# Performance work log

Measured on AMD Instinct MI355X. Metric: run time of the kernel, lower is better.

## Reference

```python
import jax, jax.numpy as jnp
import numpy as np

B, C, L = 16, 256, 2048


def setup_inputs() -> dict:
    key = jax.random.key(0)
    ks = jax.random.split(key, 7)
    s = 0.05
    return {
        "x": jax.random.normal(ks[0], (B, C, L), dtype=jnp.float32),
        "W_theta": jax.random.normal(ks[1], (C, C), dtype=jnp.float32) * s,
        "b_theta": jax.random.normal(ks[2], (C,), dtype=jnp.float32) * s,
        "W_phi": jax.random.normal(ks[3], (C, C), dtype=jnp.float32) * s,
        "b_phi": jax.random.normal(ks[4], (C,), dtype=jnp.float32) * s,
        "W_g": jax.random.normal(ks[5], (C, C), dtype=jnp.float32) * s,
        "b_g": jax.random.normal(ks[6], (C,), dtype=jnp.float32) * s,
    }


def reference(x, W_theta, b_theta, W_phi, b_phi, W_g, b_g):
    # x: [B, C, L]; 1x1 Conv1d == linear over channel dim: out[b,o,l] = W[o,c] x[b,c,l] + b[o]
    q = jnp.einsum('oc,bcl->bol', W_theta, x) + b_theta[None, :, None]  # [B,C,L]
    k = jnp.einsum('oc,bcl->bol', W_phi, x) + b_phi[None, :, None]
    v = jnp.einsum('oc,bcl->bol', W_g, x) + b_g[None, :, None]
    num_c = x.shape[1]
    # scores[b,i,j] = sum_c q[b,c,i] * k[b,c,j]
    scores = jnp.einsum('bci,bcj->bij', q, k) / jnp.sqrt(jnp.float32(num_c))  # [B,L,L]
    attn = jax.nn.softmax(scores, axis=-1)
    # out[b,i,c] = sum_j attn[b,i,j] v[b,c,j]; then permute back to [B,C,L]
    attn_out = jnp.einsum('bij,bcj->bci', attn, v)  # [B,C,L]
    return x + attn_out
```

## Files before the change

### kernel.cpp

```cpp
#include <hip/hip_runtime.h>
#include <math.h>

#define B_ 16
#define C_ 256
#define L_ 2048

using short8 = __attribute__((ext_vector_type(8))) short;
using f32x4  = __attribute__((ext_vector_type(4))) float;
using f32x16 = __attribute__((ext_vector_type(16))) float;
typedef unsigned int uint;

__device__ __forceinline__ unsigned short f2bf(float f) {
  unsigned u = __float_as_uint(f);
  return (unsigned short)((u + 0x7FFFu + ((u >> 16) & 1u)) >> 16);
}

__device__ __forceinline__ void gload16(const void* src, void* dst) {
  __builtin_amdgcn_global_load_lds(
      (const __attribute__((address_space(1))) unsigned int*)src,
      (__attribute__((address_space(3))) unsigned int*)dst, 16, 0, 0);
}

__global__ __launch_bounds__(256) void convert_w(const float* __restrict__ wt,
                                                 const float* __restrict__ wp,
                                                 const float* __restrict__ wg,
                                                 unsigned short* __restrict__ dst) {
  int i = blockIdx.x * 256 + threadIdx.x;
  dst[i]          = f2bf(wt[i]);
  dst[65536 + i]  = f2bf(wp[i]);
  dst[131072 + i] = f2bf(wg[i]);
}

__global__ __launch_bounds__(256, 2) void proj_kernel(
    const float* __restrict__ x, const unsigned short* __restrict__ wbf,
    const float* __restrict__ bth, const float* __restrict__ bph,
    const float* __restrict__ bg,
    unsigned short* __restrict__ qT, unsigned short* __restrict__ kT,
    unsigned short* __restrict__ vv)
{
  const int tid  = threadIdx.x;
  const int w    = tid >> 6;
  const int lane = tid & 63;
  const int r    = lane & 15;
  const int g    = lane >> 4;
  const int l0   = blockIdx.x * 64;
  const int b    = blockIdx.y;
  const int p    = blockIdx.z;

  __shared__ unsigned short xs[64 * 64];
  __shared__ unsigned short wsd[256 * 64];

  const unsigned short* wsrc = wbf + p * 65536;

  f32x4 acc[4][4];
#pragma unroll
  for (int mi = 0; mi < 4; ++mi)
#pragma unroll
    for (int ni = 0; ni < 4; ++ni) acc[mi][ni] = f32x4{0.f, 0.f, 0.f, 0.f};

  for (int ks = 0; ks < 4; ++ks) {
    __syncthreads();
#pragma unroll
    for (int it = 0; it < 8; ++it) {
      int d  = it * 256 + w * 64 + lane;
      int o  = d >> 3;
      int cs = d & 7;
      const unsigned short* src = wsrc + o * C_ + ks * 64 + ((cs ^ (o & 7)) << 3);
      gload16(src, (void*)(wsd + (size_t)(it * 256 + w * 64) * 8));
    }
#pragma unroll
    for (int it = 0; it < 16; ++it) {
      int l = (tid & 15) + 16 * (it & 3);
      int c = (tid >> 4) + 16 * (it >> 2);
      float xvv = x[((size_t)b * C_ + ks * 64 + c) * L_ + l0 + l];
      xs[l * 64 + (((c >> 3) ^ (l & 7)) << 3) + (c & 7)] = f2bf(xvv);
    }
    __syncthreads();

#pragma unroll
    for (int kk2 = 0; kk2 < 2; ++kk2) {
      short8 xf[4], wf[4];
#pragma unroll
      for (int i = 0; i < 4; ++i) {
        int lrow = 16 * i + r;
        xf[i] = *(const short8*)(xs + lrow * 64 + (((kk2 * 4 + g) ^ (lrow & 7)) << 3));
        int orow = 64 * w + 16 * i + r;
        wf[i] = *(const short8*)(wsd + orow * 64 + (((kk2 * 4 + g) ^ (orow & 7)) << 3));
      }
      if (p < 2) {
#pragma unroll
        for (int mi = 0; mi < 4; ++mi)
#pragma unroll
          for (int ni = 0; ni < 4; ++ni)
            acc[mi][ni] = __builtin_amdgcn_mfma_f32_16x16x32_bf16(xf[mi], wf[ni], acc[mi][ni], 0, 0, 0);
      } else {
#pragma unroll
        for (int mi = 0; mi < 4; ++mi)
#pragma unroll
          for (int ni = 0; ni < 4; ++ni)
            acc[mi][ni] = __builtin_amdgcn_mfma_f32_16x16x32_bf16(wf[mi], xf[ni], acc[mi][ni], 0, 0, 0);
      }
    }
  }

  if (p < 2) {
    unsigned short* dst = (p == 0) ? qT : kT;
    const float* bias   = (p == 0) ? bth : bph;
    const float scale   = (p == 0) ? 0.09016844005556021f : 1.0f;
#pragma unroll
    for (int ni = 0; ni < 4; ++ni) {
      int o    = 64 * w + 16 * ni + r;
      float bv = bias[o];
#pragma unroll
      for (int mi = 0; mi < 4; ++mi)
#pragma unroll
        for (int rr = 0; rr < 4; ++rr) {
          int l = l0 + 16 * mi + 4 * g + rr;
          dst[((size_t)b * L_ + l) * C_ + o] = f2bf((acc[mi][ni][rr] + bv) * scale);
        }
    }
  } else {
#pragma unroll
    for (int mi = 0; mi < 4; ++mi)
#pragma unroll
      for (int rr = 0; rr < 4; ++rr) {
        int o    = 64 * w + 16 * mi + 4 * g + rr;
        float bv = bg[o];
#pragma unroll
        for (int ni = 0; ni < 4; ++ni) {
          int l = l0 + 16 * ni + r;
          vv[((size_t)b * C_ + o) * L_ + l] = f2bf(acc[mi][ni][rr] + bv);
        }
      }
  }
}

__global__ __launch_bounds__(256, 2) void attn_kernel(
    const unsigned short* __restrict__ qT, const unsigned short* __restrict__ kT,
    const unsigned short* __restrict__ vv,
    const float* __restrict__ x, float* __restrict__ out)
{
  const int tid  = threadIdx.x;
  const int w    = tid >> 6;
  const int lane = tid & 63;
  const int l31  = lane & 31;
  const int hi   = lane >> 5;
  const int ih   = w >> 1;
  const int jh   = w & 1;

  int wg = ((blockIdx.x & 7) << 6) | (blockIdx.x >> 3);
  const int i0 = (wg & 31) * 64;
  const int b  = wg >> 5;

  __shared__ unsigned short kls[64 * 256];
  __shared__ unsigned short pls[64 * 64];
  __shared__ float lsums2[2][64];

  short8 qf[16];
  const unsigned short* qrow_p = qT + ((size_t)b * L_ + i0 + 32 * ih + l31) * C_;
#pragma unroll
  for (int ks = 0; ks < 16; ++ks)
    qf[ks] = *(const short8*)(qrow_p + ks * 16 + 8 * hi);

  f32x16 oacc[2][2];
#pragma unroll
  for (int it = 0; it < 2; ++it)
#pragma unroll
    for (int ct = 0; ct < 2; ++ct)
#pragma unroll
      for (int e = 0; e < 16; ++e) oacc[it][ct][e] = 0.f;
  float lsum = 0.f;

  const unsigned short* kTb = kT + (size_t)b * L_ * C_;
  const unsigned short* vvb = vv + (size_t)b * C_ * L_;

#pragma unroll
  for (int it = 0; it < 8; ++it) {
    int d   = it * 256 + w * 64 + lane;
    int row = d >> 5;
    int cs  = d & 31;
    gload16(kTb + (size_t)row * C_ + ((cs ^ (row & 7)) << 3),
            (void*)(kls + (size_t)(it * 256 + w * 64) * 8));
  }

  for (int jt = 0; jt < 32; ++jt) {
    const int j0 = jt * 64;
    __syncthreads();

    short8 vfr[2][4];
#pragma unroll
    for (int ct = 0; ct < 2; ++ct) {
      const unsigned short* vrow = vvb + (size_t)(l31 + 32 * ct + 64 * w) * L_ + j0 + 8 * hi;
#pragma unroll
      for (int ks = 0; ks < 4; ++ks)
        vfr[ct][ks] = *(const short8*)(vrow + 16 * ks);
    }

    f32x16 sacc;
#pragma unroll
    for (int e = 0; e < 16; ++e) sacc[e] = 0.f;
    const int jrow = l31 + 32 * jh;
#pragma unroll
    for (int ks = 0; ks < 16; ++ks) {
      short8 kf = *(const short8*)(kls + jrow * 256 + (((2 * ks + hi) ^ (jrow & 7)) << 3));
      sacc = __builtin_amdgcn_mfma_f32_32x32x16_bf16(kf, qf[ks], sacc, 0, 0, 0);
    }

    {
      const int i = l31 + 32 * ih;
#pragma unroll
      for (int q = 0; q < 4; ++q) {
        float p0 = exp2f(sacc[4 * q + 0]);
        float p1 = exp2f(sacc[4 * q + 1]);
        float p2 = exp2f(sacc[4 * q + 2]);
        float p3 = exp2f(sacc[4 * q + 3]);
        lsum += (p0 + p1) + (p2 + p3);
        uint2 d2;
        d2.x = (uint)f2bf(p0) | ((uint)f2bf(p1) << 16);
        d2.y = (uint)f2bf(p2) | ((uint)f2bf(p3) << 16);
        int slot = (4 * jh + q) ^ (i & 7);
        *(uint2*)(pls + i * 64 + slot * 8 + 4 * hi) = d2;
      }
    }
    __syncthreads();

    if (jt < 31) {
#pragma unroll
      for (int it = 0; it < 8; ++it) {
        int d   = it * 256 + w * 64 + lane;
        int row = d >> 5;
        int cs  = d & 31;
        gload16(kTb + (size_t)(j0 + 64 + row) * C_ + ((cs ^ (row & 7)) << 3),
                (void*)(kls + (size_t)(it * 256 + w * 64) * 8));
      }
    }

#pragma unroll
    for (int ks = 0; ks < 4; ++ks) {
      short8 pf[2];
#pragma unroll
      for (int it = 0; it < 2; ++it) {
        int irow = l31 + 32 * it;
        pf[it] = *(const short8*)(pls + irow * 64 + (((2 * ks + hi) ^ (irow & 7)) << 3));
      }
#pragma unroll
      for (int it = 0; it < 2; ++it)
#pragma unroll
        for (int ct = 0; ct < 2; ++ct)
          oacc[it][ct] = __builtin_amdgcn_mfma_f32_32x32x16_bf16(pf[it], vfr[ct][ks], oacc[it][ct], 0, 0, 0);
    }
  }

  lsum += __shfl_xor(lsum, 32);
  if (lane < 32) lsums2[jh][32 * ih + l31] = lsum;
  __syncthreads();

#pragma unroll
  for (int it = 0; it < 2; ++it)
#pragma unroll
    for (int q = 0; q < 4; ++q) {
      int ib = 32 * it + 8 * q + 4 * hi;
      f32x4 ls0 = *(const f32x4*)(&lsums2[0][ib]);
      f32x4 ls1 = *(const f32x4*)(&lsums2[1][ib]);
      f32x4 linv;
#pragma unroll
      for (int rr = 0; rr < 4; ++rr) linv[rr] = 1.0f / (ls0[rr] + ls1[rr]);
#pragma unroll
      for (int ct = 0; ct < 2; ++ct) {
        int c = l31 + 32 * ct + 64 * w;
        size_t base = ((size_t)b * C_ + c) * L_ + i0 + ib;
        f32x4 xv = *(const f32x4*)(x + base);
        f32x4 ov;
#pragma unroll
        for (int rr = 0; rr < 4; ++rr)
          ov[rr] = xv[rr] + oacc[it][ct][4 * q + rr] * linv[rr];
        *(f32x4*)(out + base) = ov;
      }
    }
}

extern "C" void kernel_launch(void* const* d_in, const int* in_sizes, int n_in,
                              void* d_out, int out_size, void* d_ws, size_t ws_size,
                              hipStream_t stream) {
  (void)in_sizes; (void)n_in; (void)out_size; (void)ws_size;
  const float* x   = (const float*)d_in[0];
  const float* wt  = (const float*)d_in[1];
  const float* bt  = (const float*)d_in[2];
  const float* wp  = (const float*)d_in[3];
  const float* bp  = (const float*)d_in[4];
  const float* wg  = (const float*)d_in[5];
  const float* bgg = (const float*)d_in[6];
  float* out = (float*)d_out;

  char* ws = (char*)d_ws;
  unsigned short* wbf = (unsigned short*)ws;
  unsigned short* qT  = (unsigned short*)(ws + 393216);
  unsigned short* kT  = (unsigned short*)(ws + 393216 + 16777216);
  unsigned short* vv  = (unsigned short*)(ws + 393216 + 2 * 16777216);

  convert_w<<<dim3(256), dim3(256), 0, stream>>>(wt, wp, wg, wbf);
  proj_kernel<<<dim3(32, 16, 3), dim3(256), 0, stream>>>(x, wbf, bt, bp, bgg, qT, kT, vv);
  attn_kernel<<<dim3(512), dim3(256), 0, stream>>>(qT, kT, vv, x, out);
}
```

Measured before the change: 147.0 us.

## Double-buffer K tiles in attention and fuse QKV projections into one block

The attention kernel now double-buffers the K tile in LDS, so the load of the next tile is issued at the top of each iteration and no longer waits behind the softmax barrier. It also splits the score MFMA chain into two independent accumulators, precomputes the swizzled LDS addresses, uses the hardware exp and packed bf16 convert instructions, and raises wave priority around the MFMA sections. The projection kernel loads an x tile once as bf16 into LDS and loops over the three weight matrices inside a block, replacing the three-way grid split. This cuts the number of x reads but leaves only 512 projection blocks and uses more LDS per block.

```diff
diff --git a/kernel.cpp b/kernel.cpp
--- a/kernel.cpp
+++ b/kernel.cpp
@@ -1,5 +1,4 @@
 #include <hip/hip_runtime.h>
-#include <math.h>
 
 #define B_ 16
 #define C_ 256
@@ -45,93 +44,94 @@
   const int g    = lane >> 4;
   const int l0   = blockIdx.x * 64;
   const int b    = blockIdx.y;
-  const int p    = blockIdx.z;
-
-  __shared__ unsigned short xs[64 * 64];
+
+  __shared__ unsigned short xs[64 * 256];
   __shared__ unsigned short wsd[256 * 64];
 
-  const unsigned short* wsrc = wbf + p * 65536;
+#pragma unroll
+  for (int it = 0; it < 64; ++it) {
+    int l = (tid & 15) + 16 * (it & 3);
+    int c = (tid >> 4) + 16 * (it >> 2);
+    float xvv = x[((size_t)b * C_ + c) * L_ + l0 + l];
+    xs[l * 256 + (((c >> 3) ^ (l & 7)) << 3) + (c & 7)] = f2bf(xvv);
+  }
 
   f32x4 acc[4][4];
-#pragma unroll
-  for (int mi = 0; mi < 4; ++mi)
-#pragma unroll
-    for (int ni = 0; ni < 4; ++ni) acc[mi][ni] = f32x4{0.f, 0.f, 0.f, 0.f};
-
-  for (int ks = 0; ks < 4; ++ks) {
-    __syncthreads();
-#pragma unroll
-    for (int it = 0; it < 8; ++it) {
-      int d  = it * 256 + w * 64 + lane;
-      int o  = d >> 3;
-      int cs = d & 7;
-      const unsigned short* src = wsrc + o * C_ + ks * 64 + ((cs ^ (o & 7)) << 3);
-      gload16(src, (void*)(wsd + (size_t)(it * 256 + w * 64) * 8));
-    }
-#pragma unroll
-    for (int it = 0; it < 16; ++it) {
-      int l = (tid & 15) + 16 * (it & 3);
-      int c = (tid >> 4) + 16 * (it >> 2);
-      float xvv = x[((size_t)b * C_ + ks * 64 + c) * L_ + l0 + l];
-      xs[l * 64 + (((c >> 3) ^ (l & 7)) << 3) + (c & 7)] = f2bf(xvv);
-    }
-    __syncthreads();
-
-#pragma unroll
-    for (int kk2 = 0; kk2 < 2; ++kk2) {
-      short8 xf[4], wf[4];
-#pragma unroll
-      for (int i = 0; i < 4; ++i) {
-        int lrow = 16 * i + r;
-        xf[i] = *(const short8*)(xs + lrow * 64 + (((kk2 * 4 + g) ^ (lrow & 7)) << 3));
-        int orow = 64 * w + 16 * i + r;
-        wf[i] = *(const short8*)(wsd + orow * 64 + (((kk2 * 4 + g) ^ (orow & 7)) << 3));
+  for (int p = 0; p < 3; ++p) {
+    const unsigned short* wsrc = wbf + p * 65536;
+#pragma unroll
+    for (int mi = 0; mi < 4; ++mi)
+#pragma unroll
+      for (int ni = 0; ni < 4; ++ni) acc[mi][ni] = f32x4{0.f, 0.f, 0.f, 0.f};
+
+    for (int ks = 0; ks < 4; ++ks) {
+      __syncthreads();
+#pragma unroll
+      for (int it = 0; it < 8; ++it) {
+        int o  = it * 32 + (tid >> 3);
+        int cs = tid & 7;
+        gload16(wsrc + o * C_ + ks * 64 + ((cs ^ (o & 7)) << 3),
+                (void*)(wsd + (size_t)(it * 256 + w * 64) * 8));
       }
-      if (p < 2) {
-#pragma unroll
-        for (int mi = 0; mi < 4; ++mi)
-#pragma unroll
-          for (int ni = 0; ni < 4; ++ni)
-            acc[mi][ni] = __builtin_amdgcn_mfma_f32_16x16x32_bf16(xf[mi], wf[ni], acc[mi][ni], 0, 0, 0);
-      } else {
-#pragma unroll
-        for (int mi = 0; mi < 4; ++mi)
-#pragma unroll
-          for (int ni = 0; ni < 4; ++ni)
-            acc[mi][ni] = __builtin_amdgcn_mfma_f32_16x16x32_bf16(wf[mi], xf[ni], acc[mi][ni], 0, 0, 0);
+      __syncthreads();
+
+#pragma unroll
+      for (int kk2 = 0; kk2 < 2; ++kk2) {
+        short8 xf[4], wf[4];
+#pragma unroll
+        for (int i = 0; i < 4; ++i) {
+          int lrow = 16 * i + r;
+          xf[i] = *(const short8*)(xs + lrow * 256 +
+                                   (((8 * ks + 4 * kk2 + g) ^ (lrow & 7)) << 3));
+          int orow = 64 * w + 16 * i + r;
+          wf[i] = *(const short8*)(wsd + orow * 64 + (((kk2 * 4 + g) ^ (orow & 7)) << 3));
+        }
+        if (p < 2) {
+#pragma unroll
+          for (int mi = 0; mi < 4; ++mi)
+#pragma unroll
+            for (int ni = 0; ni < 4; ++ni)
+              acc[mi][ni] = __builtin_amdgcn_mfma_f32_16x16x32_bf16(xf[mi], wf[ni], acc[mi][ni], 0, 0, 0);
+        } else {
+#pragma unroll
+          for (int mi = 0; mi < 4; ++mi)
+#pragma unroll
+            for (int ni = 0; ni < 4; ++ni)
+              acc[mi][ni] = __builtin_amdgcn_mfma_f32_16x16x32_bf16(wf[mi], xf[ni], acc[mi][ni], 0, 0, 0);
+        }
       }
     }
-  }
-
-  if (p < 2) {
-    unsigned short* dst = (p == 0) ? qT : kT;
-    const float* bias   = (p == 0) ? bth : bph;
-    const float scale   = (p == 0) ? 0.09016844005556021f : 1.0f;
-#pragma unroll
-    for (int ni = 0; ni < 4; ++ni) {
-      int o    = 64 * w + 16 * ni + r;
-      float bv = bias[o];
+
+    if (p < 2) {
+      unsigned short* dst = (p == 0) ? qT : kT;
+      const float* bias   = (p == 0) ? bth : bph;
+      const float scale   = (p == 0) ? 0.09016844005556021f : 1.0f;
+#pragma unroll
+      for (int ni = 0; ni < 4; ++ni) {
+        int o    = 64 * w + 16 * ni + r;
+        float bv = bias[o];
+#pragma unroll
+        for (int mi = 0; mi < 4; ++mi)
+#pragma unroll
+          for (int rr = 0; rr < 4; ++rr) {
+            int l = l0 + 16 * mi + 4 * g + rr;
+            dst[((size_t)b * L_ + l) * C_ + o] = f2bf((acc[mi][ni][rr] + bv) * scale);
+          }
+      }
+    } else {
 #pragma unroll
       for (int mi = 0; mi < 4; ++mi)
 #pragma unroll
         for (int rr = 0; rr < 4; ++rr) {
-          int l = l0 + 16 * mi + 4 * g + rr;
-          dst[((size_t)b * L_ + l) * C_ + o] = f2bf((acc[mi][ni][rr] + bv) * scale);
+          int o    = 64 * w + 16 * mi + 4 * g + rr;
+          float bv = bg[o];
+#pragma unroll
+          for (int ni = 0; ni < 4; ++ni) {
+            int l = l0 + 16 * ni + r;
+            vv[((size_t)b * C_ + o) * L_ + l] = f2bf(acc[mi][ni][rr] + bv);
+          }
         }
     }
-  } else {
-#pragma unroll
-    for (int mi = 0; mi < 4; ++mi)
-#pragma unroll
-      for (int rr = 0; rr < 4; ++rr) {
-        int o    = 64 * w + 16 * mi + 4 * g + rr;
-        float bv = bg[o];
-#pragma unroll
-        for (int ni = 0; ni < 4; ++ni) {
-          int l = l0 + 16 * ni + r;
-          vv[((size_t)b * C_ + o) * L_ + l] = f2bf(acc[mi][ni][rr] + bv);
-        }
-      }
   }
 }
 
@@ -152,9 +152,14 @@
   const int i0 = (wg & 31) * 64;
   const int b  = wg >> 5;
 
-  __shared__ unsigned short kls[64 * 256];
+  __shared__ unsigned short kls[2][64 * 256];
   __shared__ unsigned short pls[64 * 64];
   __shared__ float lsums2[2][64];
+  unsigned short* klsf = &kls[0][0];
+  unsigned short* plsf = pls;
+
+  const unsigned short* kTb = kT + (size_t)b * L_ * C_;
+  const unsigned short* vvb = vv + (size_t)b * C_ * L_;
 
   short8 qf[16];
   const unsigned short* qrow_p = qT + ((size_t)b * L_ + i0 + 32 * ih + l31) * C_;
@@ -162,6 +167,31 @@
   for (int ks = 0; ks < 16; ++ks)
     qf[ks] = *(const short8*)(qrow_p + ks * 16 + 8 * hi);
 
+  const int jrow = l31 + 32 * jh;
+  int kfa[16];
+#pragma unroll
+  for (int k2 = 0; k2 < 8; ++k2) {
+    kfa[2 * k2]     = jrow * 256 + (((4 * k2 + hi) ^ (jrow & 7)) << 3);
+    kfa[2 * k2 + 1] = jrow * 256 + (((4 * k2 + 2 + hi) ^ (jrow & 7)) << 3);
+  }
+  int pfa[8];
+#pragma unroll
+  for (int ks = 0; ks < 4; ++ks)
+#pragma unroll
+    for (int it = 0; it < 2; ++it)
+      pfa[2 * ks + it] = (l31 + 32 * it) * 64 + (((2 * ks + hi) ^ (l31 & 7)) << 3);
+  int pwa[4];
+  {
+    const int i = l31 + 32 * ih;
+#pragma unroll
+    for (int q = 0; q < 4; ++q)
+      pwa[q] = i * 64 + (((4 * jh + q) ^ (i & 7)) << 3) + 4 * hi;
+  }
+  const int koff0 = (tid >> 5) * 256 + (((tid & 31) ^ ((tid >> 5) & 7)) << 3);
+  int voff[2];
+#pragma unroll
+  for (int ct = 0; ct < 2; ++ct) voff[ct] = (l31 + 32 * ct + 64 * w) * L_ + 8 * hi;
+
   f32x16 oacc[2][2];
 #pragma unroll
   for (int it = 0; it < 2; ++it)
@@ -171,85 +201,83 @@
       for (int e = 0; e < 16; ++e) oacc[it][ct][e] = 0.f;
   float lsum = 0.f;
 
-  const unsigned short* kTb = kT + (size_t)b * L_ * C_;
-  const unsigned short* vvb = vv + (size_t)b * C_ * L_;
-
-#pragma unroll
-  for (int it = 0; it < 8; ++it) {
-    int d   = it * 256 + w * 64 + lane;
-    int row = d >> 5;
-    int cs  = d & 31;
-    gload16(kTb + (size_t)row * C_ + ((cs ^ (row & 7)) << 3),
-            (void*)(kls + (size_t)(it * 256 + w * 64) * 8));
-  }
-
-  for (int jt = 0; jt < 32; ++jt) {
-    const int j0 = jt * 64;
-    __syncthreads();
-
-    short8 vfr[2][4];
-#pragma unroll
-    for (int ct = 0; ct < 2; ++ct) {
-      const unsigned short* vrow = vvb + (size_t)(l31 + 32 * ct + 64 * w) * L_ + j0 + 8 * hi;
-#pragma unroll
-      for (int ks = 0; ks < 4; ++ks)
-        vfr[ct][ks] = *(const short8*)(vrow + 16 * ks);
-    }
-
-    f32x16 sacc;
-#pragma unroll
-    for (int e = 0; e < 16; ++e) sacc[e] = 0.f;
-    const int jrow = l31 + 32 * jh;
-#pragma unroll
-    for (int ks = 0; ks < 16; ++ks) {
-      short8 kf = *(const short8*)(kls + jrow * 256 + (((2 * ks + hi) ^ (jrow & 7)) << 3));
-      sacc = __builtin_amdgcn_mfma_f32_32x32x16_bf16(kf, qf[ks], sacc, 0, 0, 0);
-    }
-
-    {
-      const int i = l31 + 32 * ih;
-#pragma unroll
-      for (int q = 0; q < 4; ++q) {
-        float p0 = exp2f(sacc[4 * q + 0]);
-        float p1 = exp2f(sacc[4 * q + 1]);
-        float p2 = exp2f(sacc[4 * q + 2]);
-        float p3 = exp2f(sacc[4 * q + 3]);
-        lsum += (p0 + p1) + (p2 + p3);
-        uint2 d2;
-        d2.x = (uint)f2bf(p0) | ((uint)f2bf(p1) << 16);
-        d2.y = (uint)f2bf(p2) | ((uint)f2bf(p3) << 16);
-        int slot = (4 * jh + q) ^ (i & 7);
-        *(uint2*)(pls + i * 64 + slot * 8 + 4 * hi) = d2;
-      }
-    }
-    __syncthreads();
-
-    if (jt < 31) {
-#pragma unroll
-      for (int it = 0; it < 8; ++it) {
-        int d   = it * 256 + w * 64 + lane;
-        int row = d >> 5;
-        int cs  = d & 31;
-        gload16(kTb + (size_t)(j0 + 64 + row) * C_ + ((cs ^ (row & 7)) << 3),
-                (void*)(kls + (size_t)(it * 256 + w * 64) * 8));
-      }
-    }
-
-#pragma unroll
-    for (int ks = 0; ks < 4; ++ks) {
-      short8 pf[2];
-#pragma unroll
-      for (int it = 0; it < 2; ++it) {
-        int irow = l31 + 32 * it;
-        pf[it] = *(const short8*)(pls + irow * 64 + (((2 * ks + hi) ^ (irow & 7)) << 3));
-      }
-#pragma unroll
-      for (int it = 0; it < 2; ++it)
-#pragma unroll
-        for (int ct = 0; ct < 2; ++ct)
-          oacc[it][ct] = __builtin_amdgcn_mfma_f32_32x32x16_bf16(pf[it], vfr[ct][ks], oacc[it][ct], 0, 0, 0);
-    }
-  }
+  {
+    const unsigned short* ksrc = kTb + koff0;
+#pragma unroll
+    for (int it = 0; it < 8; ++it)
+      gload16(ksrc + it * 2048, (void*)(klsf + (it * 256 + w * 64) * 8));
+  }
+  const unsigned short* kstage = kTb + 16384;
+  const unsigned short* vbase  = vvb;
+
+#define TILE_BODY(CUR, NXT, DOSTAGE)                                               \
+  {                                                                                \
+    __syncthreads();                                                               \
+    short8 vfr[2][4];                                                              \
+    _Pragma("unroll")                                                              \
+    for (int ct = 0; ct < 2; ++ct) {                                               \
+      _Pragma("unroll")                                                            \
+      for (int ks = 0; ks < 4; ++ks)                                               \
+        vfr[ct][ks] = *(const short8*)(vbase + voff[ct] + 16 * ks);                \
+    }                                                                              \
+    if (DOSTAGE) {                                                                 \
+      const unsigned short* ksrc = kstage + koff0;                                 \
+      _Pragma("unroll")                                                            \
+      for (int it = 0; it < 8; ++it)                                               \
+        gload16(ksrc + it * 2048, (void*)(klsf + (NXT) + (it * 256 + w * 64) * 8));\
+    }                                                                              \
+    f32x16 sacc0, sacc1;                                                           \
+    _Pragma("unroll")                                                              \
+    for (int e = 0; e < 16; ++e) { sacc0[e] = 0.f; sacc1[e] = 0.f; }               \
+    __builtin_amdgcn_s_setprio(1);                                                 \
+    _Pragma("unroll")                                                              \
+    for (int k2 = 0; k2 < 8; ++k2) {                                               \
+      short8 kf0 = *(const short8*)(klsf + (CUR) + kfa[2 * k2]);                   \
+      short8 kf1 = *(const short8*)(klsf + (CUR) + kfa[2 * k2 + 1]);               \
+      sacc0 = __builtin_amdgcn_mfma_f32_32x32x16_bf16(kf0, qf[2 * k2], sacc0, 0, 0, 0);      \
+      sacc1 = __builtin_amdgcn_mfma_f32_32x32x16_bf16(kf1, qf[2 * k2 + 1], sacc1, 0, 0, 0);  \
+    }                                                                              \
+    __builtin_amdgcn_s_setprio(0);                                                 \
+    _Pragma("unroll")                                                              \
+    for (int q = 0; q < 4; ++q) {                                                  \
+      float s0 = sacc0[4 * q + 0] + sacc1[4 * q + 0];                              \
+      float s1 = sacc0[4 * q + 1] + sacc1[4 * q + 1];                              \
+      float s2 = sacc0[4 * q + 2] + sacc1[4 * q + 2];                              \
+      float s3 = sacc0[4 * q + 3] + sacc1[4 * q + 3];                              \
+      float p0, p1, p2, p3;                                                        \
+      asm("v_exp_f32 %0, %1" : "=v"(p0) : "v"(s0));                                \
+      asm("v_exp_f32 %0, %1" : "=v"(p1) : "v"(s1));                                \
+      asm("v_exp_f32 %0, %1" : "=v"(p2) : "v"(s2));                                \
+      asm("v_exp_f32 %0, %1" : "=v"(p3) : "v"(s3));                                \
+      lsum += (p0 + p1) + (p2 + p3);                                               \
+      uint dlo, dhi;                                                               \
+      asm("v_cvt_pk_bf16_f32 %0, %1, %2" : "=v"(dlo) : "v"(p0), "v"(p1));          \
+      asm("v_cvt_pk_bf16_f32 %0, %1, %2" : "=v"(dhi) : "v"(p2), "v"(p3));          \
+      uint2 d2; d2.x = dlo; d2.y = dhi;                                            \
+      *(uint2*)(plsf + pwa[q]) = d2;                                               \
+    }                                                                              \
+    __syncthreads();                                                               \
+    __builtin_amdgcn_s_setprio(1);                                                 \
+    _Pragma("unroll")                                                              \
+    for (int ks = 0; ks < 4; ++ks) {                                               \
+      short8 pf0 = *(const short8*)(plsf + pfa[2 * ks]);                           \
+      short8 pf1 = *(const short8*)(plsf + pfa[2 * ks + 1]);                       \
+      _Pragma("unroll")                                                            \
+      for (int ct = 0; ct < 2; ++ct) {                                             \
+        oacc[0][ct] = __builtin_amdgcn_mfma_f32_32x32x16_bf16(pf0, vfr[ct][ks], oacc[0][ct], 0, 0, 0); \
+        oacc[1][ct] = __builtin_amdgcn_mfma_f32_32x32x16_bf16(pf1, vfr[ct][ks], oacc[1][ct], 0, 0, 0); \
+      }                                                                            \
+    }                                                                              \
+    __builtin_amdgcn_s_setprio(0);                                                 \
+    vbase += 64;                                                                   \
+    if (DOSTAGE) kstage += 16384;                                                  \
+  }
+
+  for (int jt2 = 0; jt2 < 16; ++jt2) {
+    TILE_BODY(0, 16384, 1)
+    TILE_BODY(16384, 0, (jt2 < 15))
+  }
+#undef TILE_BODY
 
   lsum += __shfl_xor(lsum, 32);
   if (lane < 32) lsums2[jh][32 * ih + l31] = lsum;
@@ -299,6 +327,6 @@
   unsigned short* vv  = (unsigned short*)(ws + 393216 + 2 * 16777216);
 
   convert_w<<<dim3(256), dim3(256), 0, stream>>>(wt, wp, wg, wbf);
-  proj_kernel<<<dim3(32, 16, 3), dim3(256), 0, stream>>>(x, wbf, bt, bp, bgg, qT, kT, vv);
+  proj_kernel<<<dim3(32, 16), dim3(256), 0, stream>>>(x, wbf, bt, bp, bgg, qT, kT, vv);
   attn_kernel<<<dim3(512), dim3(256), 0, stream>>>(qT, kT, vv, x, out);
 }
```

New measurement: 141.7 us. 3.6% less time.
